# Performance work log

Hardware: AMD Instinct MI355X
Metric: run time of the kernel (lower is better)

Reference implementation:

```python
import jax, jax.numpy as jnp
import numpy as np

B, H, L, DIM = 4, 8, 1024, 256
D = DIM // H  # per-head dim
DEPTH, LAYER_I = 12, 1  # layer_index < depth//4 -> adjacency masking active


def _gcn(xh, adj, W):
    # One graph-convolution layer (GCN used as q/k/v projection in the repo):
    # support = x @ W per head, then aggregate with the (attention-)adjacency.
    # xh: [b,h,t,d], adj: [b,h,l,t], W: [d,d] -> [b,h,l,d]
    return jnp.einsum('bhlt,bhtd->bhld', adj, xh @ W)


def _split_heads(x):
    # 'b t (h d) -> b h t d'
    b, t, _ = x.shape
    return x.reshape(b, t, H, D).transpose(0, 2, 1, 3)


def _merge_heads(v):
    # 'b h t d -> b t (h d)'
    b, h, t, d = v.shape
    return v.transpose(0, 2, 1, 3).reshape(b, t, h * d)


def setup_inputs() -> dict:
    key = jax.random.key(0)
    ks = jax.random.split(key, 9)
    x = jax.random.normal(ks[0], (B, L, DIM), jnp.float32)
    resize_x = jax.random.normal(ks[1], (B, L, DIM), jnpp := jnp.float32) if False else jax.random.normal(ks[1], (B, L, DIM), jnp.float32)
    eye = jnp.eye(L, dtype=jnp.float32)[None, None]  # self-loops so no all-masked rows
    adj = jnp.clip((jax.random.uniform(ks[2], (B, H, L, L)) < 0.1).astype(jnp.float32) + eye, 0.0, 1.0)
    adj_resize = jnp.clip((jax.random.uniform(ks[3], (B, H, L, L)) < 0.1).astype(jnp.float32) + eye, 0.0, 1.0)
    s = D ** -0.5
    Wq = jax.random.normal(ks[4], (D, D), jnp.float32) * s
    Wk = jax.random.normal(ks[5], (D, D), jnp.float32) * s
    Wv = jax.random.normal(ks[6], (D, D), jnp.float32) * s
    R = jax.random.normal(ks[7], (H, H), jnp.float32)  # 'randomatrix' head-mixing param
    Wp = jax.random.normal(ks[8], (DIM, DIM), jnp.float32) * (DIM ** -0.5)  # proj_v (no bias)
    return {'x': x, 'resize_x': resize_x, 'adj': adj, 'adj_resize': adj_resize,
            'Wq': Wq, 'Wk': Wk, 'Wv': Wv, 'R': R, 'Wp': Wp}


def reference(x, resize_x, adj, adj_resize, Wq, Wk, Wv, R, Wp):
    scale = DIM ** -0.5  # note: torch code scales by dim**-0.5 (full dim, not d_head)
    xh = _split_heads(x)          # [b,h,l,d]
    rxh = _split_heads(resize_x)  # [b,h,t,d]
    q = _gcn(xh, adj, Wq)         # [b,h,l,d]
    k = _gcn(rxh, adj_resize, Wk)  # [b,h,t,d]
    attn = jnp.einsum('bhld,bhtd->bhlt', q, k) * scale
    attn = jax.nn.leaky_relu(attn, negative_slope=0.01)
    # cross-head mixing with learned HxH matrix: out[b,i] = sum_h R[i,h]*attn[b,h]
    attn = jnp.einsum('ih,bhlt->bilt', R, attn)
    if LAYER_I < DEPTH // 4:
        attn = jnp.where(adj > 0, attn, -jnp.inf)
    A = jax.nn.softmax(attn, axis=-1)                      # rep_adj
    Ar = jax.nn.softmax(A.transpose(0, 1, 3, 2), axis=-1)  # dual softmax on transpose
    v = _merge_heads(_gcn(xh, A, Wv))
    out = jax.nn.gelu(v, approximate=False) @ Wp
    vr = _merge_heads(_gcn(rxh, Ar, Wv))
    out_resize = jax.nn.gelu(vr, approximate=False) @ Wp
    return out, out_resize, A, Ar
```

## Files before the change

### kernel.cpp

```cpp
#include <hip/hip_runtime.h>
#include <hip/hip_bf16.h>
#include <math.h>

#define BB 4
#define HH 8
#define LL 1024
#define DD 32
#define DIMM 256

typedef unsigned short u16;
typedef unsigned int u32;
typedef short bf16x8 __attribute__((ext_vector_type(8)));
typedef float f32x4 __attribute__((ext_vector_type(4)));

__device__ __forceinline__ float bu2f(u16 s) {
  union { unsigned int u; float f; } cv; cv.u = ((unsigned int)s) << 16; return cv.f;
}
__device__ __forceinline__ u16 f2bu(float f) {
  union { float f; unsigned int u; } cv; cv.f = f;
  unsigned int u = cv.u;
  u += 0x7FFFu + ((u >> 16) & 1u);
  return (u16)(u >> 16);
}
__device__ __forceinline__ short f2bs(float f) {
  return (short)__bfloat16_as_ushort(__float2bfloat16(f));
}

__global__ __launch_bounds__(256) void k_proj(
    const float* __restrict__ x, const float* __restrict__ rx,
    const float* __restrict__ Wq, const float* __restrict__ Wk, const float* __restrict__ Wv,
    u16* __restrict__ xqT_hi, u16* __restrict__ xqT_lo,
    u16* __restrict__ xkT_hi, u16* __restrict__ xkT_lo,
    u16* __restrict__ xvT_hi, u16* __restrict__ xvrT_hi) {
  __shared__ float wq[32][32], wk[32][32], wv[32][32];
  __shared__ float xs[8][32], rxs[8][32];
  __shared__ float tq_[32][9], tk_[32][9], tv_[32][9], tvr_[32][9];
  int tid = threadIdx.x, bid = blockIdx.x;
  int chunk = bid & 127, h = (bid >> 7) & 7, b = bid >> 10;
  int t0 = chunk << 3;
  for (int i = tid; i < 1024; i += 256) {
    int r = i >> 5, c = i & 31;
    wq[r][c] = Wq[i]; wk[r][c] = Wk[i]; wv[r][c] = Wv[i];
  }
  int d = tid & 31, tl = tid >> 5;
  size_t xoff = ((size_t)b * LL + t0 + tl) * DIMM + h * 32 + d;
  xs[tl][d]  = x[xoff];
  rxs[tl][d] = rx[xoff];
  __syncthreads();
  float aq = 0.f, ak = 0.f, av = 0.f, ar = 0.f;
#pragma unroll
  for (int dp = 0; dp < 32; ++dp) {
    float xv_ = xs[tl][dp], rv_ = rxs[tl][dp];
    aq += xv_ * wq[dp][d];
    ak += rv_ * wk[dp][d];
    av += xv_ * wv[dp][d];
    ar += rv_ * wv[dp][d];
  }
  tq_[d][tl] = aq; tk_[d][tl] = ak; tv_[d][tl] = av; tvr_[d][tl] = ar;
  __syncthreads();
  int d2 = tid >> 3, t2 = tid & 7;
  size_t obase = ((size_t)((b * HH + h) * DD + d2)) * LL + t0 + t2;
  {
    float v = tq_[d2][t2]; u16 hi = f2bu(v);
    xqT_hi[obase] = hi; xqT_lo[obase] = f2bu(v - bu2f(hi));
  }
  {
    float v = tk_[d2][t2]; u16 hi = f2bu(v);
    xkT_hi[obase] = hi; xkT_lo[obase] = f2bu(v - bu2f(hi));
  }
  xvT_hi[obase]  = f2bu(tv_[d2][t2]);
  xvrT_hi[obase] = f2bu(tvr_[d2][t2]);
}

template<int PREC, int OUT_SPLIT, int WRITE_BITS>
__global__ __launch_bounds__(256) void k_wmat2(
    const float* __restrict__ wA, const float* __restrict__ wB,
    const u16* __restrict__ sAh, const u16* __restrict__ sAl,
    const u16* __restrict__ sBh, const u16* __restrict__ sBl,
    float* __restrict__ dA, float* __restrict__ dB,
    u16* __restrict__ dAhi, u16* __restrict__ dAlo,
    u16* __restrict__ dBhi, u16* __restrict__ dBlo,
    u32* __restrict__ bits) {
  int tid = threadIdx.x, bid = blockIdx.x;
  int sel = bid >> 9;
  const float* w  = sel ? wB : wA;
  const u16* sh   = sel ? sBh : sAh;
  const u16* sl   = sel ? sBl : sAl;
  float* dst      = sel ? dB : dA;
  u16* dhi        = sel ? dBhi : dAhi;
  u16* dlo        = sel ? dBlo : dAlo;
  int b2 = bid & 511;
  int lc = b2 & 15, bh = b2 >> 4;
  int wave = tid >> 6, lane = tid & 63;
  int l0 = (lc << 6) + (wave << 4);
  int col = lane & 15, g = lane >> 4;
  const float* wrow = w + ((size_t)bh * LL + l0 + col) * LL + (g << 3);
  const u16* b0h = sh + ((size_t)bh * DD + col) * LL + (g << 3);
  const u16* b1h = b0h + 16 * LL;
  const u16* b0l = PREC == 2 ? sl + ((size_t)bh * DD + col) * LL + (g << 3) : nullptr;
  const u16* b1l = PREC == 2 ? b0l + 16 * LL : nullptr;
  unsigned char* bytep = nullptr;
  if (WRITE_BITS && sel == 0)
    bytep = (unsigned char*)(bits + (size_t)bh * 32 * LL + l0 + col) + g;
  f32x4 acc0 = {0.f, 0.f, 0.f, 0.f}, acc1 = {0.f, 0.f, 0.f, 0.f};
#pragma unroll 4
  for (int t0 = 0; t0 < LL; t0 += 32) {
    f32x4 wa = *(const f32x4*)(wrow + t0);
    f32x4 wb = *(const f32x4*)(wrow + t0 + 4);
    bf16x8 whi;
#pragma unroll
    for (int i = 0; i < 4; ++i) {
      whi[i]     = f2bs(wa[i]);
      whi[i + 4] = f2bs(wb[i]);
    }
    if (WRITE_BITS && sel == 0) {
      unsigned int byte = 0;
#pragma unroll
      for (int i = 0; i < 4; ++i) {
        byte |= (wa[i] > 0.f ? 1u : 0u) << i;
        byte |= (wb[i] > 0.f ? 1u : 0u) << (4 + i);
      }
      bytep[(size_t)(t0 >> 5) * (LL * 4)] = (unsigned char)byte;
    }
    bf16x8 s0h = *(const bf16x8*)(b0h + t0);
    bf16x8 s1h = *(const bf16x8*)(b1h + t0);
    acc0 = __builtin_amdgcn_mfma_f32_16x16x32_bf16(whi, s0h, acc0, 0, 0, 0);
    acc1 = __builtin_amdgcn_mfma_f32_16x16x32_bf16(whi, s1h, acc1, 0, 0, 0);
    if (PREC == 2) {
      bf16x8 s0l = *(const bf16x8*)(b0l + t0);
      bf16x8 s1l = *(const bf16x8*)(b1l + t0);
      acc0 = __builtin_amdgcn_mfma_f32_16x16x32_bf16(whi, s0l, acc0, 0, 0, 0);
      acc1 = __builtin_amdgcn_mfma_f32_16x16x32_bf16(whi, s1l, acc1, 0, 0, 0);
    }
  }
#pragma unroll
  for (int i = 0; i < 4; ++i) {
    size_t o = ((size_t)bh * LL + l0 + (g << 2) + i) * DD;
    if (OUT_SPLIT) {
      float v0 = acc0[i]; u16 h0 = f2bu(v0);
      dhi[o + col] = h0; dlo[o + col] = f2bu(v0 - bu2f(h0));
      float v1 = acc1[i]; u16 h1 = f2bu(v1);
      dhi[o + 16 + col] = h1; dlo[o + 16 + col] = f2bu(v1 - bu2f(h1));
    } else {
      dst[o + col] = acc0[i];
      dst[o + 16 + col] = acc1[i];
    }
  }
}

__global__ __launch_bounds__(256) void k_logits_mfma(
    const u16* __restrict__ qh, const u16* __restrict__ ql,
    const u16* __restrict__ kh, const u16* __restrict__ kl,
    const float* __restrict__ Rm, const u32* __restrict__ bits,
    float* __restrict__ M) {
  __shared__ float Rlds[8][8];
  __shared__ float mtile[4][16 * 17];
  int tid = threadIdx.x, bid = blockIdx.x;
  int lb = bid & 15, tb = (bid >> 4) & 15, b = bid >> 8;
  int wave = tid >> 6, lane = tid & 63;
  int l0 = (lb << 6) + (wave << 4);
  int tbase = tb << 6;
  int idx16 = lane & 15, g = lane >> 4;
  if (tid < 64) Rlds[tid >> 3][tid & 7] = Rm[tid];
  bf16x8 qfh[8], qfl[8];
#pragma unroll
  for (int h = 0; h < 8; ++h) {
    size_t off = ((size_t)(b * HH + h) * LL + l0 + idx16) * DD + (g << 3);
    qfh[h] = *(const bf16x8*)(qh + off);
    qfl[h] = *(const bf16x8*)(ql + off);
  }
  __syncthreads();
  int rr_ = lane >> 2, c0 = (lane & 3) << 2;
  for (int tt = 0; tt < 4; ++tt) {
    int t = tbase + (tt << 4);
    f32x4 S[8];
#pragma unroll
    for (int h = 0; h < 8; ++h) {
      size_t koff = ((size_t)(b * HH + h) * LL + t + idx16) * DD + (g << 3);
      bf16x8 bh_ = *(const bf16x8*)(kh + koff);
      bf16x8 bl_ = *(const bf16x8*)(kl + koff);
      f32x4 s = {0.f, 0.f, 0.f, 0.f};
      s = __builtin_amdgcn_mfma_f32_16x16x32_bf16(qfh[h], bh_, s, 0, 0, 0);
      s = __builtin_amdgcn_mfma_f32_16x16x32_bf16(qfl[h], bh_, s, 0, 0, 0);
      s = __builtin_amdgcn_mfma_f32_16x16x32_bf16(qfh[h], bl_, s, 0, 0, 0);
      S[h] = s;
    }
#pragma unroll
    for (int h = 0; h < 8; ++h)
#pragma unroll
      for (int e = 0; e < 4; ++e) {
        float v = S[h][e] * 0.0625f;
        S[h][e] = (v > 0.f) ? v : 0.01f * v;
      }
    int word = t >> 5;
    int bitpos = ((tt & 1) << 4) + idx16;
#pragma unroll
    for (int i = 0; i < 8; ++i) {
      float rr8[8];
#pragma unroll
      for (int h = 0; h < 8; ++h) rr8[h] = Rlds[i][h];
      const u32* bp = bits + ((size_t)(b * HH + i) * 32 + word) * LL + l0 + (g << 2);
      u32 mw0 = bp[0], mw1 = bp[1], mw2 = bp[2], mw3 = bp[3];
      float m_[4];
#pragma unroll
      for (int e = 0; e < 4; ++e) {
        float acc = 0.f;
#pragma unroll
        for (int h = 0; h < 8; ++h) acc += rr8[h] * S[h][e];
        u32 mw = (e == 0) ? mw0 : (e == 1) ? mw1 : (e == 2) ? mw2 : mw3;
        m_[e] = ((mw >> bitpos) & 1u) ? acc : -INFINITY;
      }
#pragma unroll
      for (int e = 0; e < 4; ++e)
        mtile[wave][((g << 2) + e) * 17 + idx16] = m_[e];
      float4 v4;
      v4.x = mtile[wave][rr_ * 17 + c0 + 0];
      v4.y = mtile[wave][rr_ * 17 + c0 + 1];
      v4.z = mtile[wave][rr_ * 17 + c0 + 2];
      v4.w = mtile[wave][rr_ * 17 + c0 + 3];
      *(float4*)(M + ((size_t)(b * HH + i) * LL + l0 + rr_) * LL + t + c0) = v4;
    }
  }
}

__global__ __launch_bounds__(256) void k_norm2v(
    float* __restrict__ A, const u16* __restrict__ xvT,
    float* __restrict__ colpart, float* __restrict__ vb) {
  __shared__ u16 Ast[32][1032];
  int tid = threadIdx.x, bid = blockIdx.x;
  int ch = bid & 31, bh = bid >> 5;
  int wave = tid >> 6, lane = tid & 63;
  float4 colA[4];
#pragma unroll
  for (int j = 0; j < 4; ++j) colA[j] = make_float4(0.f, 0.f, 0.f, 0.f);
  for (int rr = 0; rr < 8; ++rr) {
    int row = (rr << 2) + wave;
    int l = (ch << 5) + row;
    float4* Ap = (float4*)(A + ((size_t)bh * LL + l) * LL);
    float4 v[4];
#pragma unroll
    for (int j = 0; j < 4; ++j) v[j] = Ap[lane + (j << 6)];
    float mx = -INFINITY;
#pragma unroll
    for (int j = 0; j < 4; ++j)
      mx = fmaxf(mx, fmaxf(fmaxf(v[j].x, v[j].y), fmaxf(v[j].z, v[j].w)));
#pragma unroll
    for (int o = 32; o > 0; o >>= 1) mx = fmaxf(mx, __shfl_xor(mx, o, 64));
    float sm = 0.f;
#pragma unroll
    for (int j = 0; j < 4; ++j) {
      v[j].x = __expf(v[j].x - mx); v[j].y = __expf(v[j].y - mx);
      v[j].z = __expf(v[j].z - mx); v[j].w = __expf(v[j].w - mx);
      sm += v[j].x + v[j].y + v[j].z + v[j].w;
    }
#pragma unroll
    for (int o = 32; o > 0; o >>= 1) sm += __shfl_xor(sm, o, 64);
    float inv = 1.0f / sm;
#pragma unroll
    for (int j = 0; j < 4; ++j) {
      v[j].x *= inv; v[j].y *= inv; v[j].z *= inv; v[j].w *= inv;
      colA[j].x += __expf(v[j].x); colA[j].y += __expf(v[j].y);
      colA[j].z += __expf(v[j].z); colA[j].w += __expf(v[j].w);
      Ap[lane + (j << 6)] = v[j];
      int c4 = (lane + (j << 6)) << 2;
      *(short4*)&Ast[row][c4] =
          make_short4(f2bs(v[j].x), f2bs(v[j].y), f2bs(v[j].z), f2bs(v[j].w));
    }
  }
  __syncthreads();
  int idx16 = lane & 15, g = lane >> 4;
  int Mt = wave >> 1, Nt = wave & 1;
  f32x4 acc = {0.f, 0.f, 0.f, 0.f};
  const u16* bbase = xvT + ((size_t)bh * DD + Nt * 16 + idx16) * LL;
#pragma unroll 4
  for (int kc = 0; kc < 32; ++kc) {
    bf16x8 af = *(const bf16x8*)&Ast[(Mt << 4) + idx16][(kc << 5) + (g << 3)];
    bf16x8 bfr = *(const bf16x8*)(bbase + (kc << 5) + (g << 3));
    acc = __builtin_amdgcn_mfma_f32_16x16x32_bf16(af, bfr, acc, 0, 0, 0);
  }
#pragma unroll
  for (int e = 0; e < 4; ++e)
    vb[((size_t)bh * LL + (ch << 5) + (Mt << 4) + (g << 2) + e) * DD + Nt * 16 + idx16] = acc[e];
  __syncthreads();
  float* cf = (float*)&Ast[0][0];
#pragma unroll
  for (int j = 0; j < 4; ++j)
    *(float4*)&cf[wave * 1024 + (j << 8) + (lane << 2)] = colA[j];
  __syncthreads();
  float4 s = make_float4(0.f, 0.f, 0.f, 0.f);
#pragma unroll
  for (int w = 0; w < 4; ++w) {
    float4 t = *(const float4*)&cf[w * 1024 + (tid << 2)];
    s.x += t.x; s.y += t.y; s.z += t.z; s.w += t.w;
  }
  ((float4*)(colpart + ((size_t)bh * 32 + ch) * LL))[tid] = s;
}

__global__ __launch_bounds__(256) void k_arv(
    const float* __restrict__ A, const float* __restrict__ colpart,
    const u16* __restrict__ xvrT, float* __restrict__ Ar, float* __restrict__ vrb) {
  __shared__ float tile[64][65];
  int tid = threadIdx.x, bid = blockIdx.x;
  int tix = bid & 15, bh = bid >> 4;
  int t0 = tix << 6;
  int c = tid & 63, w4 = tid >> 6;
  int idx16 = c & 15, g = (c >> 4) & 3;
  float cs = 0.f;
  {
    const float* cp = colpart + (size_t)bh * 32 * LL + t0 + c;
#pragma unroll
    for (int chk = 0; chk < 32; ++chk) cs += cp[chk * LL];
  }
  float invc = 1.0f / cs;
  f32x4 acc0 = {0.f, 0.f, 0.f, 0.f}, acc1 = {0.f, 0.f, 0.f, 0.f};
  for (int tiy = 0; tiy < 16; ++tiy) {
    int l0 = tiy << 6;
    const float* Ab = A + ((size_t)bh * LL + l0) * LL + t0;
#pragma unroll
    for (int rr = 0; rr < 16; ++rr) {
      int li = (rr << 2) + w4;
      tile[li][c] = __expf(Ab[(size_t)li * LL + c]) * invc;
    }
    __syncthreads();
    float* Arb = Ar + ((size_t)bh * LL + t0) * LL + l0;
#pragma unroll
    for (int rr = 0; rr < 16; ++rr) {
      int ti = (rr << 2) + w4;
      Arb[(size_t)ti * LL + c] = tile[c][ti];
    }
#pragma unroll
    for (int kc = 0; kc < 2; ++kc) {
      bf16x8 af;
#pragma unroll
      for (int j = 0; j < 8; ++j)
        af[j] = f2bs(tile[(kc << 5) + (g << 3) + j][(w4 << 4) + idx16]);
      const u16* bp = xvrT + ((size_t)bh * DD + idx16) * LL + l0 + (kc << 5) + (g << 3);
      bf16x8 b0 = *(const bf16x8*)bp;
      bf16x8 b1 = *(const bf16x8*)(bp + 16 * LL);
      acc0 = __builtin_amdgcn_mfma_f32_16x16x32_bf16(af, b0, acc0, 0, 0, 0);
      acc1 = __builtin_amdgcn_mfma_f32_16x16x32_bf16(af, b1, acc1, 0, 0, 0);
    }
    __syncthreads();
  }
#pragma unroll
  for (int e = 0; e < 4; ++e) {
    size_t o = ((size_t)bh * LL + t0 + (w4 << 4) + (g << 2) + e) * DD;
    vrb[o + idx16] = acc0[e];
    vrb[o + 16 + idx16] = acc1[e];
  }
}

__global__ __launch_bounds__(256) void k_out2(
    const float* __restrict__ vb, const float* __restrict__ vrb,
    const float* __restrict__ Wp,
    float* __restrict__ out, float* __restrict__ outr) {
  __shared__ float g_s[16 * 256];
  __shared__ float wp_s[32 * 256];
  int tid = threadIdx.x, bid = blockIdx.x;
  int sel = bid >> 8;
  const float* vbuf = sel ? vrb : vb;
  float* o = sel ? outr : out;
  int b2 = bid & 255;
  int lt = b2 & 63, b = b2 >> 6;
  int l0 = lt << 4;
  int h = tid >> 5, dd = tid & 31;
#pragma unroll
  for (int r = 0; r < 16; ++r) {
    float v = vbuf[(((size_t)b * HH + h) * LL + l0 + r) * DD + dd];
    g_s[r * 256 + tid] = 0.5f * v * (1.0f + erff(v * 0.70710678118654752f));
  }
  float acc[16];
#pragma unroll
  for (int r = 0; r < 16; ++r) acc[r] = 0.f;
  for (int jc = 0; jc < 8; ++jc) {
    __syncthreads();
#pragma unroll
    for (int u = 0; u < 8; ++u) {
      int idx = tid + (u << 8);
      int j = idx >> 6, c4 = idx & 63;
      float4 v = *(const float4*)(Wp + (size_t)(jc * 32 + j) * DIMM + (c4 << 2));
      *(float4*)&wp_s[j * 256 + (c4 << 2)] = v;
    }
    __syncthreads();
#pragma unroll
    for (int j = 0; j < 32; ++j) {
      float wv = wp_s[j * 256 + tid];
      int jj = (jc << 5) + j;
#pragma unroll
      for (int r = 0; r < 16; ++r)
        acc[r] += g_s[r * 256 + jj] * wv;
    }
  }
#pragma unroll
  for (int r = 0; r < 16; ++r)
    o[((size_t)b * LL + l0 + r) * DIMM + tid] = acc[r];
}

extern "C" void kernel_launch(void* const* d_in, const int* in_sizes, int n_in,
                              void* d_out, int out_size, void* d_ws, size_t ws_size,
                              hipStream_t stream) {
  const float* x    = (const float*)d_in[0];
  const float* rx   = (const float*)d_in[1];
  const float* adj  = (const float*)d_in[2];
  const float* adjr = (const float*)d_in[3];
  const float* Wq   = (const float*)d_in[4];
  const float* Wk   = (const float*)d_in[5];
  const float* Wv   = (const float*)d_in[6];
  const float* Rm   = (const float*)d_in[7];
  const float* Wp   = (const float*)d_in[8];

  const size_t NE = (size_t)BB * HH * LL * DD;

  float* out  = (float*)d_out;
  float* outr = out + NE;
  float* A    = outr + NE;
  float* Ar   = A + (size_t)BB * HH * LL * LL;

  u16* q_hi   = (u16*)(Ar);
  u16* q_lo   = q_hi + NE;
  u16* k_hi   = q_lo + NE;
  u16* k_lo   = k_hi + NE;
  u16* xqT_hi = k_lo + NE;
  u16* xqT_lo = xqT_hi + NE;
  u16* xkT_hi = xqT_lo + NE;
  u16* xkT_lo = xkT_hi + NE;
  u16* xvT_hi  = (u16*)out;
  u16* xvrT_hi = (u16*)outr;

  float* wsf    = (float*)d_ws;
  float* vb     = wsf;
  float* vrb    = wsf + NE;
  float* colpart = wsf + 2 * NE;
  u32* adjbits  = (u32*)(wsf + 3 * NE);

  k_proj<<<4096, 256, 0, stream>>>(x, rx, Wq, Wk, Wv,
                                   xqT_hi, xqT_lo, xkT_hi, xkT_lo,
                                   xvT_hi, xvrT_hi);
  k_wmat2<2,1,1><<<1024, 256, 0, stream>>>(adj, adjr,
                                           xqT_hi, xqT_lo, xkT_hi, xkT_lo,
                                           nullptr, nullptr,
                                           q_hi, q_lo, k_hi, k_lo, adjbits);
  k_logits_mfma<<<1024, 256, 0, stream>>>(q_hi, q_lo, k_hi, k_lo, Rm, adjbits, A);
  k_norm2v<<<1024, 256, 0, stream>>>(A, xvT_hi, colpart, vb);
  k_arv<<<512, 256, 0, stream>>>(A, colpart, xvrT_hi, Ar, vrb);
  k_out2<<<512, 256, 0, stream>>>(vb, vrb, Wp, out, outr);
}
```

Before: 385.6 us.

## Halve k_arv column tile to double grid and vectorize A loads

The transpose/exp/MFMA kernel for Ar and vr now handles 32 columns per block instead of 64, doubling the grid to 1024 blocks. Each wave owns one 16x16 output tile instead of two. A is read with float4 loads, and the column-sum reduction is split across all threads through shared memory. The 1/colsum scaling moves to the store and fragment-build steps. More blocks should fill the CUs better, but the Ar writes now cover only 32 rows per tile, and the A rows read are 128 bytes wide instead of 256.

```diff
diff --git a/kernel.cpp b/kernel.cpp
--- a/kernel.cpp
+++ b/kernel.cpp
@@ -296,57 +296,72 @@
   ((float4*)(colpart + ((size_t)bh * 32 + ch) * LL))[tid] = s;
 }
 
-__global__ __launch_bounds__(256) void k_arv(
+__global__ __launch_bounds__(256) void k_arv2(
     const float* __restrict__ A, const float* __restrict__ colpart,
     const u16* __restrict__ xvrT, float* __restrict__ Ar, float* __restrict__ vrb) {
-  __shared__ float tile[64][65];
-  int tid = threadIdx.x, bid = blockIdx.x;
-  int tix = bid & 15, bh = bid >> 4;
-  int t0 = tix << 6;
-  int c = tid & 63, w4 = tid >> 6;
-  int idx16 = c & 15, g = (c >> 4) & 3;
-  float cs = 0.f;
+  __shared__ float tile[64][33];
+  __shared__ float cpart[8][32];
+  __shared__ float cinv[32];
+  int tid = threadIdx.x, bid = blockIdx.x;
+  int tix = bid & 31, bh = bid >> 5;
+  int t0 = tix << 5;
+  int wave = tid >> 6, lane = tid & 63;
+  int idx16 = lane & 15, g = lane >> 4;
+  int mt = wave >> 1, nt = wave & 1;
   {
-    const float* cp = colpart + (size_t)bh * 32 * LL + t0 + c;
-#pragma unroll
-    for (int chk = 0; chk < 32; ++chk) cs += cp[chk * LL];
-  }
-  float invc = 1.0f / cs;
-  f32x4 acc0 = {0.f, 0.f, 0.f, 0.f}, acc1 = {0.f, 0.f, 0.f, 0.f};
+    int tl = tid & 31, grp = tid >> 5;
+    float p = 0.f;
+#pragma unroll
+    for (int j = 0; j < 4; ++j)
+      p += colpart[((size_t)bh * 32 + (grp << 2) + j) * LL + t0 + tl];
+    cpart[grp][tl] = p;
+  }
+  __syncthreads();
+  if (tid < 32) {
+    float cs = 0.f;
+#pragma unroll
+    for (int i = 0; i < 8; ++i) cs += cpart[i][tid];
+    cinv[tid] = 1.0f / cs;
+  }
+  __syncthreads();
+  float myinv = cinv[(mt << 4) + idx16];
+  f32x4 acc = {0.f, 0.f, 0.f, 0.f};
+  int c2 = tid & 63, r4 = tid >> 6;
+  const u16* bp0 = xvrT + ((size_t)bh * DD + (nt << 4) + idx16) * LL;
   for (int tiy = 0; tiy < 16; ++tiy) {
     int l0 = tiy << 6;
-    const float* Ab = A + ((size_t)bh * LL + l0) * LL + t0;
-#pragma unroll
-    for (int rr = 0; rr < 16; ++rr) {
-      int li = (rr << 2) + w4;
-      tile[li][c] = __expf(Ab[(size_t)li * LL + c]) * invc;
+#pragma unroll
+    for (int u = 0; u < 2; ++u) {
+      int f4 = tid + (u << 8);
+      int li = f4 >> 3, c4 = (f4 & 7) << 2;
+      float4 v = *(const float4*)(A + ((size_t)bh * LL + l0 + li) * LL + t0 + c4);
+      tile[li][c4 + 0] = __expf(v.x);
+      tile[li][c4 + 1] = __expf(v.y);
+      tile[li][c4 + 2] = __expf(v.z);
+      tile[li][c4 + 3] = __expf(v.w);
     }
     __syncthreads();
     float* Arb = Ar + ((size_t)bh * LL + t0) * LL + l0;
 #pragma unroll
-    for (int rr = 0; rr < 16; ++rr) {
-      int ti = (rr << 2) + w4;
-      Arb[(size_t)ti * LL + c] = tile[c][ti];
+    for (int rr = 0; rr < 8; ++rr) {
+      int ti = (rr << 2) + r4;
+      Arb[(size_t)ti * LL + c2] = tile[c2][ti] * cinv[ti];
     }
 #pragma unroll
     for (int kc = 0; kc < 2; ++kc) {
       bf16x8 af;
 #pragma unroll
       for (int j = 0; j < 8; ++j)
-        af[j] = f2bs(tile[(kc << 5) + (g << 3) + j][(w4 << 4) + idx16]);
-      const u16* bp = xvrT + ((size_t)bh * DD + idx16) * LL + l0 + (kc << 5) + (g << 3);
-      bf16x8 b0 = *(const bf16x8*)bp;
-      bf16x8 b1 = *(const bf16x8*)(bp + 16 * LL);
-      acc0 = __builtin_amdgcn_mfma_f32_16x16x32_bf16(af, b0, acc0, 0, 0, 0);
-      acc1 = __builtin_amdgcn_mfma_f32_16x16x32_bf16(af, b1, acc1, 0, 0, 0);
+        af[j] = f2bs(tile[(kc << 5) + (g << 3) + j][(mt << 4) + idx16] * myinv);
+      bf16x8 bfr = *(const bf16x8*)(bp0 + l0 + (kc << 5) + (g << 3));
+      acc = __builtin_amdgcn_mfma_f32_16x16x32_bf16(af, bfr, acc, 0, 0, 0);
     }
     __syncthreads();
   }
 #pragma unroll
   for (int e = 0; e < 4; ++e) {
-    size_t o = ((size_t)bh * LL + t0 + (w4 << 4) + (g << 2) + e) * DD;
-    vrb[o + idx16] = acc0[e];
-    vrb[o + 16 + idx16] = acc1[e];
+    size_t o = ((size_t)bh * LL + t0 + (mt << 4) + (g << 2) + e) * DD;
+    vrb[o + (nt << 4) + idx16] = acc[e];
   }
 }
 
@@ -442,6 +457,6 @@
                                            q_hi, q_lo, k_hi, k_lo, adjbits);
   k_logits_mfma<<<1024, 256, 0, stream>>>(q_hi, q_lo, k_hi, k_lo, Rm, adjbits, A);
   k_norm2v<<<1024, 256, 0, stream>>>(A, xvT_hi, colpart, vb);
-  k_arv<<<512, 256, 0, stream>>>(A, colpart, xvrT_hi, Ar, vrb);
+  k_arv2<<<1024, 256, 0, stream>>>(A, colpart, xvrT_hi, Ar, vrb);
   k_out2<<<512, 256, 0, stream>>>(vb, vrb, Wp, out, outr);
 }
```

Result: no change. 383.0 us (-0.7%).
